# Optimization experiments

Measured on AMD Instinct MI355X. Metric: run time of the kernel, lower is better.

Reference implementation:

```python
import jax, jax.numpy as jnp
import numpy as np

B, N, C, H = 16, 4096, 1024, 8
D = C // H  # head dim = 128
EPS = 1e-5


def layernorm(x, gamma, beta):
    mu = jnp.mean(x, axis=-1, keepdims=True)
    var = jnp.mean(jnp.square(x - mu), axis=-1, keepdims=True)
    return (x - mu) * jax.lax.rsqrt(var + EPS) * gamma + beta


def setup_inputs() -> dict:
    key = jax.random.key(0)
    ks = jax.random.split(key, 5)
    w_std = C ** -0.5
    return {
        "class_feature": jax.random.normal(ks[0], (1, 1, C), dtype=jnp.float32),
        "features": jax.random.normal(ks[1], (B, N, C), dtype=jnp.float32),
        "q_gamma": jnp.ones((C,), jnp.float32),
        "q_beta": jnp.zeros((C,), jnp.float32),
        "Wq": jax.random.normal(ks[2], (C, C), dtype=jnp.float32) * w_std,
        "kv_gamma": jnp.ones((C,), jnp.float32),
        "kv_beta": jnp.zeros((C,), jnp.float32),
        "Wkv": jax.random.normal(ks[3], (2 * C, C), dtype=jnp.float32) * w_std,
        "proj_W": jax.random.normal(ks[4], (C, C), dtype=jnp.float32) * w_std,
        "proj_b": jnp.zeros((C,), jnp.float32),
    }


def reference(class_feature, features, q_gamma, q_beta, Wq,
              kv_gamma, kv_beta, Wkv, proj_W, proj_b):
    b, n, c = features.shape
    scale = c ** -0.5  # NOTE: original scales by input_size^-0.5, not head_dim^-0.5
    cf = jnp.broadcast_to(class_feature, (b, 1, c))  # repeat(B,1,1)

    # q branch: LN + Linear (no bias); single query token per batch
    q = layernorm(cf, q_gamma, q_beta) @ Wq.T            # (B,1,C)
    q = q.reshape(b, H, D)                               # (B,H,D)

    # kv branch: LN + Linear -> split into k,v per head
    kv = layernorm(features, kv_gamma, kv_beta) @ Wkv.T  # (B,N,2C)
    kv = kv.reshape(b, n, 2, H, D)
    k = kv[:, :, 0]                                      # (B,N,H,D)
    v = kv[:, :, 1]                                      # (B,N,H,D)

    # single-query attention per head
    attn = jnp.einsum('bhd,bnhd->bhn', q * scale, k)     # (B,H,N)
    attn = jax.nn.softmax(attn, axis=-1)
    agg = jnp.einsum('bhn,bnhd->bhd', attn, v)           # (B,H,D)
    agg = agg.reshape(b, 1, c)

    return cf + agg @ proj_W.T + proj_b
```

## Files before the change

kernel.cpp:

```cpp
#include <hip/hip_runtime.h>
#include <math.h>


#define BB 16
#define NN 4096
#define CC 1024
#define HH 8
#define DD 128
#define CHUNKS 32
#define RPB 128
#define TPT 4
#define NT 32

constexpr float EPS_ = 1e-5f;
constexpr float SCALE_ = 0.03125f;

typedef float v2f __attribute__((ext_vector_type(2)));

__device__ __forceinline__ void pkfma(v2f& d, v2f a, v2f b) {
  asm("v_pk_fma_f32 %0, %1, %2, %0" : "+v"(d) : "v"(a), "v"(b));
}
__device__ __forceinline__ void pkadd(v2f& d, v2f a) {
  asm("v_pk_add_f32 %0, %1, %0" : "+v"(d) : "v"(a));
}
__device__ __forceinline__ v2f lo2(const float4& f) { return v2f{f.x, f.y}; }
__device__ __forceinline__ v2f hi2(const float4& f) { return v2f{f.z, f.w}; }

__device__ __forceinline__ float wsum(float v) {
#pragma unroll
  for (int o = 32; o; o >>= 1) v += __shfl_xor(v, o, 64);
  return v;
}

__device__ __forceinline__ float dpp_sum63(float v) {
  int t;
  t = __builtin_amdgcn_update_dpp(0, __float_as_int(v), 0x111, 0xf, 0xf, true);  v += __int_as_float(t);
  t = __builtin_amdgcn_update_dpp(0, __float_as_int(v), 0x112, 0xf, 0xf, true);  v += __int_as_float(t);
  t = __builtin_amdgcn_update_dpp(0, __float_as_int(v), 0x114, 0xf, 0xf, true);  v += __int_as_float(t);
  t = __builtin_amdgcn_update_dpp(0, __float_as_int(v), 0x118, 0xf, 0xf, true);  v += __int_as_float(t);
  t = __builtin_amdgcn_update_dpp(0, __float_as_int(v), 0x142, 0xa, 0xf, false); v += __int_as_float(t);
  t = __builtin_amdgcn_update_dpp(0, __float_as_int(v), 0x143, 0xc, 0xf, false); v += __int_as_float(t);
  return v;
}

__device__ __forceinline__ float rsum_u(float v) {
  return __int_as_float(__builtin_amdgcn_readlane(__float_as_int(dpp_sum63(v)), 63));
}

__device__ __forceinline__ float dot4(const float4& a, const float4& b) {
  return a.x * b.x + a.y * b.y + a.z * b.z + a.w * b.w;
}
__device__ __forceinline__ float sum4(const float4& a) {
  return (a.x + a.y) + (a.z + a.w);
}

__device__ __forceinline__ void bar_lgkm() {
  asm volatile("s_waitcnt lgkmcnt(0)" ::: "memory");
  __builtin_amdgcn_sched_barrier(0);
  __builtin_amdgcn_s_barrier();
  __builtin_amdgcn_sched_barrier(0);
}

__global__ __launch_bounds__(256) void k0b(const float* __restrict__ cf,
                                           const float* __restrict__ g,
                                           const float* __restrict__ be,
                                           const float* __restrict__ Wq,
                                           float* __restrict__ qvec) {
  __shared__ __align__(16) float lnbuf[CC];
  __shared__ float red[8];
  int t = threadIdx.x, lane = t & 63, wid = t >> 6;
  float x[4];
  float s = 0.f, s2 = 0.f;
#pragma unroll
  for (int j = 0; j < 4; ++j) {
    x[j] = cf[t * 4 + j];
    s += x[j];
    s2 += x[j] * x[j];
  }
  s = wsum(s);
  s2 = wsum(s2);
  if (lane == 0) { red[wid] = s; red[4 + wid] = s2; }
  __syncthreads();
  float S = red[0] + red[1] + red[2] + red[3];
  float S2 = red[4] + red[5] + red[6] + red[7];
  float mu = S * (1.f / CC);
  float rstd = rsqrtf(S2 * (1.f / CC) - mu * mu + EPS_);
#pragma unroll
  for (int j = 0; j < 4; ++j)
    lnbuf[t * 4 + j] = (x[j] - mu) * rstd * g[t * 4 + j] + be[t * 4 + j];
  __syncthreads();
  int j = blockIdx.x * 4 + wid;
  const float4* wr = (const float4*)(Wq + (size_t)j * CC);
  const float4* l4 = (const float4*)lnbuf;
  float a = 0.f;
#pragma unroll
  for (int k = 0; k < 4; ++k) a += dot4(wr[lane + 64 * k], l4[lane + 64 * k]);
  a = wsum(a);
  if (lane == 0) qvec[j] = a;
}

__global__ __launch_bounds__(256) void k0c(const float* __restrict__ qvec,
                                           const float* __restrict__ Wkv,
                                           const float* __restrict__ kvg,
                                           float* __restrict__ qW,
                                           float* __restrict__ qWg) {
  int h = blockIdx.x >> 4;
  int c0 = (blockIdx.x & 15) * 64;
  int t = threadIdx.x, cl = t & 63, g = t >> 6;
  float a = 0.f;
#pragma unroll 8
  for (int d = g * 32; d < g * 32 + 32; ++d)
    a += qvec[h * DD + d] * Wkv[((size_t)(h * DD + d)) * CC + c0 + cl];
  __shared__ float red[4][64];
  red[g][cl] = a;
  __syncthreads();
  if (t < 64) {
    float v = (red[0][t] + red[1][t] + red[2][t] + red[3][t]) * SCALE_;
    qW[h * CC + c0 + t] = v;
    qWg[h * CC + c0 + t] = v * kvg[c0 + t];
  }
}

__global__ __launch_bounds__(256, 2) void kfused(
    const float* __restrict__ x, const float* __restrict__ qWg,
    const float* __restrict__ qW, const float* __restrict__ kvb,
    float* __restrict__ part_s, float* __restrict__ part_meu) {
  __shared__ __align__(16) float xbuf[2][TPT * CC];
  __shared__ __align__(8) float mr_lds[2][TPT][2];

  const int t = threadIdx.x, lane = t & 63, wid = t >> 6;
  const int chunk = blockIdx.x, b = blockIdx.y;
  const int bc = b * CHUNKS + chunk;
  const int h0 = wid * 2;

  const float* gx = x + ((size_t)b * NN + (size_t)chunk * RPB) * CC;
  const int sl = wid * 256 + lane;

  float4 pf[4];
  {
    const float4* g0 = (const float4*)gx;
#pragma unroll
    for (int k = 0; k < 4; ++k) pf[k] = g0[sl + 64 * k];
  }

  float4 qw0[4], qw1[4];
  {
    const float4* a0 = (const float4*)(qWg + (size_t)h0 * CC);
    const float4* a1 = (const float4*)(qWg + (size_t)(h0 + 1) * CC);
#pragma unroll
    for (int k = 0; k < 4; ++k) {
      qw0[k] = a0[lane + 64 * k];
      qw1[k] = a1[lane + 64 * k];
    }
  }
  float qs0, qs1, qb0, qb1;
  {
    float s0 = 0.f, s1 = 0.f, t0 = 0.f, t1 = 0.f;
    const float4* w0 = (const float4*)(qW + (size_t)h0 * CC);
    const float4* w1 = (const float4*)(qW + (size_t)(h0 + 1) * CC);
    const float4* b4 = (const float4*)kvb;
#pragma unroll
    for (int k = 0; k < 4; ++k) {
      s0 += sum4(qw0[k]);
      s1 += sum4(qw1[k]);
      float4 bt = b4[lane + 64 * k];
      t0 += dot4(w0[lane + 64 * k], bt);
      t1 += dot4(w1[lane + 64 * k], bt);
    }
    qs0 = rsum_u(s0);
    qs1 = rsum_u(s1);
    qb0 = rsum_u(t0);
    qb1 = rsum_u(t1);
  }

  v2f acc0[8], acc1[8];
#pragma unroll
  for (int k = 0; k < 8; ++k) {
    acc0[k] = v2f{0.f, 0.f};
    acc1[k] = v2f{0.f, 0.f};
  }
  float e0 = 0.f, e1 = 0.f, un0 = 0.f, un1 = 0.f;

  for (int tl = 0; tl < NT; ++tl) {
    const int cur = tl & 1;
    {
      v2f sv = v2f{0.f, 0.f}, sv2 = v2f{0.f, 0.f};
#pragma unroll
      for (int k = 0; k < 4; ++k) {
        v2f plo = lo2(pf[k]), phi = hi2(pf[k]);
        pkadd(sv, plo);
        pkadd(sv, phi);
        pkfma(sv2, plo, plo);
        pkfma(sv2, phi, phi);
      }
      float ls = sv.x + sv.y;
      float ls2 = sv2.x + sv2.y;
      {
        float4* dst = (float4*)xbuf[cur];
#pragma unroll
        for (int k = 0; k < 4; ++k) dst[sl + 64 * k] = pf[k];
      }
      ls = dpp_sum63(ls);
      ls2 = dpp_sum63(ls2);
      if (lane == 63) {
        float mu = ls * (1.f / CC);
        float rs = rsqrtf(ls2 * (1.f / CC) - mu * mu + EPS_);
        mr_lds[cur][wid][0] = mu;
        mr_lds[cur][wid][1] = rs;
      }
    }
    if (tl + 1 < NT) {
      const float4* gn = (const float4*)(gx + (size_t)(tl + 1) * (TPT * CC));
#pragma unroll
      for (int k = 0; k < 4; ++k) pf[k] = gn[sl + 64 * k];
    }
    bar_lgkm();

    const float4* xb4 = (const float4*)xbuf[cur];
#pragma unroll
    for (int r = 0; r < TPT; ++r) {
      float4 x0 = xb4[r * 256 + lane];
      float4 x1 = xb4[r * 256 + lane + 64];
      float4 x2 = xb4[r * 256 + lane + 128];
      float4 x3 = xb4[r * 256 + lane + 192];
      v2f xl0 = lo2(x0), xh0 = hi2(x0), xl1 = lo2(x1), xh1 = hi2(x1);
      v2f xl2 = lo2(x2), xh2 = hi2(x2), xl3 = lo2(x3), xh3 = hi2(x3);
      v2f d0v = v2f{0.f, 0.f}, d1v = v2f{0.f, 0.f};
      pkfma(d0v, lo2(qw0[0]), xl0); pkfma(d0v, hi2(qw0[0]), xh0);
      pkfma(d0v, lo2(qw0[1]), xl1); pkfma(d0v, hi2(qw0[1]), xh1);
      pkfma(d0v, lo2(qw0[2]), xl2); pkfma(d0v, hi2(qw0[2]), xh2);
      pkfma(d0v, lo2(qw0[3]), xl3); pkfma(d0v, hi2(qw0[3]), xh3);
      pkfma(d1v, lo2(qw1[0]), xl0); pkfma(d1v, hi2(qw1[0]), xh0);
      pkfma(d1v, lo2(qw1[1]), xl1); pkfma(d1v, hi2(qw1[1]), xh1);
      pkfma(d1v, lo2(qw1[2]), xl2); pkfma(d1v, hi2(qw1[2]), xh2);
      pkfma(d1v, lo2(qw1[3]), xl3); pkfma(d1v, hi2(qw1[3]), xh3);
      float D0 = rsum_u(d0v.x + d0v.y);
      float D1 = rsum_u(d1v.x + d1v.y);
      float2 mr = *(const float2*)mr_lds[cur][r];
      float mu = mr.x, rs = mr.y;
      float l0 = fminf(rs * (D0 - mu * qs0) + qb0, 75.f);
      float l1 = fminf(rs * (D1 - mu * qs1) + qb1, 75.f);
      float p0 = __expf(l0), p1 = __expf(l1);
      float w0 = p0 * rs, w1 = p1 * rs;
      e0 += p0; e1 += p1;
      un0 += w0 * mu; un1 += w1 * mu;
      v2f w0v = v2f{w0, w0}, w1v = v2f{w1, w1};
      pkfma(acc0[0], w0v, xl0); pkfma(acc0[1], w0v, xh0);
      pkfma(acc0[2], w0v, xl1); pkfma(acc0[3], w0v, xh1);
      pkfma(acc0[4], w0v, xl2); pkfma(acc0[5], w0v, xh2);
      pkfma(acc0[6], w0v, xl3); pkfma(acc0[7], w0v, xh3);
      pkfma(acc1[0], w1v, xl0); pkfma(acc1[1], w1v, xh0);
      pkfma(acc1[2], w1v, xl1); pkfma(acc1[3], w1v, xh1);
      pkfma(acc1[4], w1v, xl2); pkfma(acc1[5], w1v, xh2);
      pkfma(acc1[6], w1v, xl3); pkfma(acc1[7], w1v, xh3);
    }
  }

  float4* p0 = (float4*)(part_s + ((size_t)bc * HH + h0) * CC);
  float4* p1 = (float4*)(part_s + ((size_t)bc * HH + h0 + 1) * CC);
#pragma unroll
  for (int k = 0; k < 4; ++k) {
    p0[64 * k + lane] = make_float4(acc0[2 * k].x, acc0[2 * k].y,
                                    acc0[2 * k + 1].x, acc0[2 * k + 1].y);
    p1[64 * k + lane] = make_float4(acc1[2 * k].x, acc1[2 * k].y,
                                    acc1[2 * k + 1].x, acc1[2 * k + 1].y);
  }
  if (lane == 0) {
    float* pm = part_meu + ((size_t)bc * HH + h0) * 2;
    pm[0] = e0; pm[1] = un0;
    pm[2] = e1; pm[3] = un1;
  }
}

__global__ __launch_bounds__(256) void kmerge(
    const float* __restrict__ part_s, const float* __restrict__ part_meu,
    const float* __restrict__ kvg, const float* __restrict__ kvb,
    float* __restrict__ s) {
  int h = blockIdx.x >> 2, q = blockIdx.x & 3, b = blockIdx.y;
  int col = q * 256 + threadIdx.x;
  float E = 0.f, UN = 0.f, a = 0.f;
  for (int ch = 0; ch < CHUNKS; ++ch) {
    const float* pm = part_meu + (((size_t)b * CHUNKS + ch) * HH + h) * 2;
    E += pm[0];
    UN += pm[1];
    a += part_s[(((size_t)b * CHUNKS + ch) * HH + h) * CC + col];
  }
  float inv = 1.f / E;
  s[((size_t)b * HH + h) * CC + col] = kvg[col] * (a - UN) * inv + kvb[col];
}

__global__ __launch_bounds__(256) void k5(const float* __restrict__ Wkv,
                                          const float* __restrict__ s,
                                          float* __restrict__ agg) {
  int lane = threadIdx.x & 63;
  int j = blockIdx.x * 4 + (threadIdx.x >> 6);
  int h = j >> 7;
  const float4* wr = (const float4*)(Wkv + ((size_t)(CC + j)) * CC);
  float4 wv[4];
#pragma unroll
  for (int k = 0; k < 4; ++k) wv[k] = wr[lane + 64 * k];
  for (int b = 0; b < BB; ++b) {
    const float4* s4 = (const float4*)(s + ((size_t)(b * HH + h)) * CC);
    float a = 0.f;
#pragma unroll
    for (int k = 0; k < 4; ++k) a += dot4(wv[k], s4[lane + 64 * k]);
    a = wsum(a);
    if (lane == 0) agg[b * CC + j] = a;
  }
}

__global__ __launch_bounds__(256) void k6(const float* __restrict__ pW,
                                          const float* __restrict__ agg,
                                          const float* __restrict__ cf,
                                          const float* __restrict__ pb,
                                          float* __restrict__ out) {
  int lane = threadIdx.x & 63;
  int j = blockIdx.x * 4 + (threadIdx.x >> 6);
  const float4* wr = (const float4*)(pW + (size_t)j * CC);
  float4 wv[4];
#pragma unroll
  for (int k = 0; k < 4; ++k) wv[k] = wr[lane + 64 * k];
  for (int b = 0; b < BB; ++b) {
    const float4* a4 = (const float4*)(agg + (size_t)b * CC);
    float a = 0.f;
#pragma unroll
    for (int k = 0; k < 4; ++k) a += dot4(wv[k], a4[lane + 64 * k]);
    a = wsum(a);
    if (lane == 0) out[b * CC + j] = cf[j] + a + pb[j];
  }
}

constexpr size_t WS_QVEC = 0;
constexpr size_t WS_QW   = 1024;
constexpr size_t WS_QWG  = 9216;
constexpr size_t WS_S    = 17408;
constexpr size_t WS_AGG  = 148480;
constexpr size_t WS_PMEU = 164864;
constexpr size_t WS_PART = 173056;

extern "C" void kernel_launch(void* const* d_in, const int* in_sizes, int n_in,
                              void* d_out, int out_size, void* d_ws, size_t ws_size,
                              hipStream_t stream) {
  const float* cf = (const float*)d_in[0];
  const float* x = (const float*)d_in[1];
  const float* qg = (const float*)d_in[2];
  const float* qb = (const float*)d_in[3];
  const float* Wq = (const float*)d_in[4];
  const float* kvg = (const float*)d_in[5];
  const float* kvb = (const float*)d_in[6];
  const float* Wkv = (const float*)d_in[7];
  const float* pW = (const float*)d_in[8];
  const float* pb = (const float*)d_in[9];
  float* ws = (float*)d_ws;
  float* out = (float*)d_out;

  k0b<<<256, 256, 0, stream>>>(cf, qg, qb, Wq, ws + WS_QVEC);
  k0c<<<128, 256, 0, stream>>>(ws + WS_QVEC, Wkv, kvg, ws + WS_QW, ws + WS_QWG);
  kfused<<<dim3(CHUNKS, BB), 256, 0, stream>>>(x, ws + WS_QWG, ws + WS_QW, kvb,
                                               ws + WS_PART, ws + WS_PMEU);
  kmerge<<<dim3(HH * 4, BB), 256, 0, stream>>>(ws + WS_PART, ws + WS_PMEU, kvg, kvb,
                                               ws + WS_S);
  k5<<<256, 256, 0, stream>>>(Wkv, ws + WS_S, ws + WS_AGG);
  k6<<<256, 256, 0, stream>>>(pW, ws + WS_AGG, cf, pb, out);
}
```

Measured before the change: 102.4 us.

## Stage feature tiles via direct global-to-LDS loads and double tile rows

Replaces the register prefetch followed by an LDS store with __builtin_amdgcn_global_load_lds, which DMAs each 8-row tile straight into the alternate LDS buffer. Tile height goes from 4 to 8 rows, so there are half as many iterations and barriers, and each wave now computes LayerNorm statistics for two rows read back from LDS. The aim is to free VGPRs and the VALU/LDS-write work spent copying the tile, and to cut per-tile sync overhead. In exchange, LDS use doubles to 64KB per block, which could hurt the two-blocks-per-CU occupancy, and the vmcnt wait at the top of each iteration may expose load latency.

```diff
diff --git a/kernel.cpp b/kernel.cpp
--- a/kernel.cpp
+++ b/kernel.cpp
@@ -9,8 +9,8 @@
 #define DD 128
 #define CHUNKS 32
 #define RPB 128
-#define TPT 4
-#define NT 32
+#define TPT 8
+#define NT 16
 
 constexpr float EPS_ = 1e-5f;
 constexpr float SCALE_ = 0.03125f;
@@ -59,6 +59,26 @@
   __builtin_amdgcn_sched_barrier(0);
   __builtin_amdgcn_s_barrier();
   __builtin_amdgcn_sched_barrier(0);
+}
+
+__device__ __forceinline__ void wait_vm0() {
+  asm volatile("s_waitcnt vmcnt(0)" ::: "memory");
+  __builtin_amdgcn_sched_barrier(0);
+}
+
+__device__ __forceinline__ void stage_tile(const float* gsrc, float* lbase,
+                                           int ra, int lane) {
+#pragma unroll
+  for (int r = 0; r < 2; ++r) {
+#pragma unroll
+    for (int k = 0; k < 4; ++k) {
+      const char* g = (const char*)gsrc + (ra + r) * 4096 + k * 1024 + lane * 16;
+      char* l = (char*)lbase + (ra + r) * 4096 + k * 1024;
+      __builtin_amdgcn_global_load_lds(
+          (const __attribute__((address_space(1))) void*)g,
+          (__attribute__((address_space(3))) void*)l, 16, 0, 0);
+    }
+  }
 }
 
 __global__ __launch_bounds__(256) void k0b(const float* __restrict__ cf,
@@ -132,16 +152,10 @@
   const int chunk = blockIdx.x, b = blockIdx.y;
   const int bc = b * CHUNKS + chunk;
   const int h0 = wid * 2;
+  const int ra = wid * 2;
 
   const float* gx = x + ((size_t)b * NN + (size_t)chunk * RPB) * CC;
-  const int sl = wid * 256 + lane;
-
-  float4 pf[4];
-  {
-    const float4* g0 = (const float4*)gx;
-#pragma unroll
-    for (int k = 0; k < 4; ++k) pf[k] = g0[sl + 64 * k];
-  }
+  stage_tile(gx, xbuf[0], ra, lane);
 
   float4 qw0[4], qw1[4];
   {
@@ -183,38 +197,43 @@
 
   for (int tl = 0; tl < NT; ++tl) {
     const int cur = tl & 1;
+
+    wait_vm0();
+
     {
-      v2f sv = v2f{0.f, 0.f}, sv2 = v2f{0.f, 0.f};
+      const float4* xb4 = (const float4*)xbuf[cur];
+      v2f svA = v2f{0.f, 0.f}, svA2 = v2f{0.f, 0.f};
+      v2f svB = v2f{0.f, 0.f}, svB2 = v2f{0.f, 0.f};
 #pragma unroll
       for (int k = 0; k < 4; ++k) {
-        v2f plo = lo2(pf[k]), phi = hi2(pf[k]);
-        pkadd(sv, plo);
-        pkadd(sv, phi);
-        pkfma(sv2, plo, plo);
-        pkfma(sv2, phi, phi);
+        float4 xa = xb4[ra * 256 + lane + 64 * k];
+        float4 xb = xb4[(ra + 1) * 256 + lane + 64 * k];
+        v2f al = lo2(xa), ah = hi2(xa), bl = lo2(xb), bh = hi2(xb);
+        pkadd(svA, al); pkadd(svA, ah);
+        pkfma(svA2, al, al); pkfma(svA2, ah, ah);
+        pkadd(svB, bl); pkadd(svB, bh);
+        pkfma(svB2, bl, bl); pkfma(svB2, bh, bh);
       }
-      float ls = sv.x + sv.y;
-      float ls2 = sv2.x + sv2.y;
-      {
-        float4* dst = (float4*)xbuf[cur];
-#pragma unroll
-        for (int k = 0; k < 4; ++k) dst[sl + 64 * k] = pf[k];
+      float lsA = dpp_sum63(svA.x + svA.y);
+      float lsA2 = dpp_sum63(svA2.x + svA2.y);
+      float lsB = dpp_sum63(svB.x + svB.y);
+      float lsB2 = dpp_sum63(svB2.x + svB2.y);
+      if (lane == 63) {
+        float muA = lsA * (1.f / CC);
+        float rsA = rsqrtf(lsA2 * (1.f / CC) - muA * muA + EPS_);
+        float muB = lsB * (1.f / CC);
+        float rsB = rsqrtf(lsB2 * (1.f / CC) - muB * muB + EPS_);
+        mr_lds[cur][ra][0] = muA;
+        mr_lds[cur][ra][1] = rsA;
+        mr_lds[cur][ra + 1][0] = muB;
+        mr_lds[cur][ra + 1][1] = rsB;
       }
-      ls = dpp_sum63(ls);
-      ls2 = dpp_sum63(ls2);
-      if (lane == 63) {
-        float mu = ls * (1.f / CC);
-        float rs = rsqrtf(ls2 * (1.f / CC) - mu * mu + EPS_);
-        mr_lds[cur][wid][0] = mu;
-        mr_lds[cur][wid][1] = rs;
-      }
-    }
-    if (tl + 1 < NT) {
-      const float4* gn = (const float4*)(gx + (size_t)(tl + 1) * (TPT * CC));
-#pragma unroll
-      for (int k = 0; k < 4; ++k) pf[k] = gn[sl + 64 * k];
-    }
+    }
+
     bar_lgkm();
+
+    if (tl + 1 < NT)
+      stage_tile(gx + (size_t)(tl + 1) * (TPT * CC), xbuf[cur ^ 1], ra, lane);
 
     const float4* xb4 = (const float4*)xbuf[cur];
 #pragma unroll
```

Result: slower. 107.8 us (+5.3%).

## Stage feature tiles via direct global-to-LDS loads with triple-buffered pipeline

Applied to the files above, without the earlier changes.

Replaces the register-staged prefetch (global load into registers, then LDS store) with global_load_lds DMA straight into shared memory. Shared buffers go from two to three so tile tl+2 can be in flight while tile tl is computed, with vmcnt waits as the guard. The LayerNorm statistics are now read back from LDS rather than taken from registers. This removes the register round-trip and the LDS store instructions and frees VGPRs. In exchange it uses more LDS per block, which may affect the two-blocks-per-CU occupancy, and it depends on correct vmcnt accounting.

```diff
diff --git a/kernel.cpp b/kernel.cpp
--- a/kernel.cpp
+++ b/kernel.cpp
@@ -59,6 +59,27 @@
   __builtin_amdgcn_sched_barrier(0);
   __builtin_amdgcn_s_barrier();
   __builtin_amdgcn_sched_barrier(0);
+}
+
+__device__ __forceinline__ void wait_vm4() {
+  asm volatile("s_waitcnt vmcnt(4)" ::: "memory");
+  __builtin_amdgcn_sched_barrier(0);
+}
+__device__ __forceinline__ void wait_vm0() {
+  asm volatile("s_waitcnt vmcnt(0)" ::: "memory");
+  __builtin_amdgcn_sched_barrier(0);
+}
+
+__device__ __forceinline__ void stage_tile(const float* gsrc, float* lbase,
+                                           int wid, int lane) {
+#pragma unroll
+  for (int k = 0; k < 4; ++k) {
+    const char* g = (const char*)gsrc + wid * 4096 + k * 1024 + lane * 16;
+    char* l = (char*)lbase + wid * 4096 + k * 1024;
+    __builtin_amdgcn_global_load_lds(
+        (const __attribute__((address_space(1))) void*)g,
+        (__attribute__((address_space(3))) void*)l, 16, 0, 0);
+  }
 }
 
 __global__ __launch_bounds__(256) void k0b(const float* __restrict__ cf,
@@ -125,8 +146,8 @@
     const float* __restrict__ x, const float* __restrict__ qWg,
     const float* __restrict__ qW, const float* __restrict__ kvb,
     float* __restrict__ part_s, float* __restrict__ part_meu) {
-  __shared__ __align__(16) float xbuf[2][TPT * CC];
-  __shared__ __align__(8) float mr_lds[2][TPT][2];
+  __shared__ __align__(16) float xbuf[3][TPT * CC];
+  __shared__ __align__(8) float mr_lds[3][TPT][2];
 
   const int t = threadIdx.x, lane = t & 63, wid = t >> 6;
   const int chunk = blockIdx.x, b = blockIdx.y;
@@ -134,14 +155,8 @@
   const int h0 = wid * 2;
 
   const float* gx = x + ((size_t)b * NN + (size_t)chunk * RPB) * CC;
-  const int sl = wid * 256 + lane;
-
-  float4 pf[4];
-  {
-    const float4* g0 = (const float4*)gx;
-#pragma unroll
-    for (int k = 0; k < 4; ++k) pf[k] = g0[sl + 64 * k];
-  }
+  stage_tile(gx, xbuf[0], wid, lane);
+  stage_tile(gx + TPT * CC, xbuf[1], wid, lane);
 
   float4 qw0[4], qw1[4];
   {
@@ -181,27 +196,24 @@
   }
   float e0 = 0.f, e1 = 0.f, un0 = 0.f, un1 = 0.f;
 
+  int cur = 0;
   for (int tl = 0; tl < NT; ++tl) {
-    const int cur = tl & 1;
+    if (tl < NT - 1) wait_vm4(); else wait_vm0();
+
     {
+      const float4* xr = (const float4*)xbuf[cur] + wid * 256;
       v2f sv = v2f{0.f, 0.f}, sv2 = v2f{0.f, 0.f};
 #pragma unroll
       for (int k = 0; k < 4; ++k) {
-        v2f plo = lo2(pf[k]), phi = hi2(pf[k]);
-        pkadd(sv, plo);
-        pkadd(sv, phi);
-        pkfma(sv2, plo, plo);
-        pkfma(sv2, phi, phi);
+        float4 xa = xr[lane + 64 * k];
+        v2f al = lo2(xa), ah = hi2(xa);
+        pkadd(sv, al);
+        pkadd(sv, ah);
+        pkfma(sv2, al, al);
+        pkfma(sv2, ah, ah);
       }
-      float ls = sv.x + sv.y;
-      float ls2 = sv2.x + sv2.y;
-      {
-        float4* dst = (float4*)xbuf[cur];
-#pragma unroll
-        for (int k = 0; k < 4; ++k) dst[sl + 64 * k] = pf[k];
-      }
-      ls = dpp_sum63(ls);
-      ls2 = dpp_sum63(ls2);
+      float ls = dpp_sum63(sv.x + sv.y);
+      float ls2 = dpp_sum63(sv2.x + sv2.y);
       if (lane == 63) {
         float mu = ls * (1.f / CC);
         float rs = rsqrtf(ls2 * (1.f / CC) - mu * mu + EPS_);
@@ -209,12 +221,14 @@
         mr_lds[cur][wid][1] = rs;
       }
     }
-    if (tl + 1 < NT) {
-      const float4* gn = (const float4*)(gx + (size_t)(tl + 1) * (TPT * CC));
-#pragma unroll
-      for (int k = 0; k < 4; ++k) pf[k] = gn[sl + 64 * k];
-    }
+
     bar_lgkm();
+
+    if (tl + 2 < NT) {
+      int slot = cur + 2;
+      if (slot >= 3) slot -= 3;
+      stage_tile(gx + (size_t)(tl + 2) * (TPT * CC), xbuf[slot], wid, lane);
+    }
 
     const float4* xb4 = (const float4*)xbuf[cur];
 #pragma unroll
@@ -254,6 +268,7 @@
       pkfma(acc1[4], w1v, xl2); pkfma(acc1[5], w1v, xh2);
       pkfma(acc1[6], w1v, xl3); pkfma(acc1[7], w1v, xh3);
     }
+    cur = (cur + 1 == 3) ? 0 : cur + 1;
   }
 
   float4* p0 = (float4*)(part_s + ((size_t)bc * HH + h0) * CC);
```

Measured after the change: 106.3 us. +3.8%, slower.

## Fuse chunk merge with V-projection into one kernel using LDS

Applied to the files above, without the earlier changes.

Merges the per-chunk partial sums kernel and the Wkv value-projection kernel into one launch per (head, batch). The merged s vector stays in shared memory instead of going through global workspace, which removes one launch and the s round trip. In exchange, each block re-reads its head's 128 Wkv rows, so V weights are read 16 times (once per batch) instead of once, and the grid shrinks to 128 blocks. The reduction also switches to a DPP-based sum whose result lands in lane 63.

```diff
diff --git a/kernel.cpp b/kernel.cpp
--- a/kernel.cpp
+++ b/kernel.cpp
@@ -272,40 +272,51 @@
   }
 }
 
-__global__ __launch_bounds__(256) void kmerge(
+__global__ __launch_bounds__(256) void kmerge5(
     const float* __restrict__ part_s, const float* __restrict__ part_meu,
     const float* __restrict__ kvg, const float* __restrict__ kvb,
-    float* __restrict__ s) {
-  int h = blockIdx.x >> 2, q = blockIdx.x & 3, b = blockIdx.y;
-  int col = q * 256 + threadIdx.x;
-  float E = 0.f, UN = 0.f, a = 0.f;
+    const float* __restrict__ Wkv, float* __restrict__ agg) {
+  __shared__ __align__(16) float s_lds[CC];
+  const int h = blockIdx.x, b = blockIdx.y;
+  const int t = threadIdx.x, lane = t & 63, wid = t >> 6;
+
+  float E = 0.f, UN = 0.f;
   for (int ch = 0; ch < CHUNKS; ++ch) {
     const float* pm = part_meu + (((size_t)b * CHUNKS + ch) * HH + h) * 2;
     E += pm[0];
     UN += pm[1];
-    a += part_s[(((size_t)b * CHUNKS + ch) * HH + h) * CC + col];
   }
   float inv = 1.f / E;
-  s[((size_t)b * HH + h) * CC + col] = kvg[col] * (a - UN) * inv + kvb[col];
-}
-
-__global__ __launch_bounds__(256) void k5(const float* __restrict__ Wkv,
-                                          const float* __restrict__ s,
-                                          float* __restrict__ agg) {
-  int lane = threadIdx.x & 63;
-  int j = blockIdx.x * 4 + (threadIdx.x >> 6);
-  int h = j >> 7;
-  const float4* wr = (const float4*)(Wkv + ((size_t)(CC + j)) * CC);
-  float4 wv[4];
-#pragma unroll
-  for (int k = 0; k < 4; ++k) wv[k] = wr[lane + 64 * k];
-  for (int b = 0; b < BB; ++b) {
-    const float4* s4 = (const float4*)(s + ((size_t)(b * HH + h)) * CC);
+
+  float4 a4 = make_float4(0.f, 0.f, 0.f, 0.f);
+  for (int ch = 0; ch < CHUNKS; ++ch) {
+    const float4* ps =
+        (const float4*)(part_s + (((size_t)b * CHUNKS + ch) * HH + h) * CC);
+    float4 v = ps[t];
+    a4.x += v.x; a4.y += v.y; a4.z += v.z; a4.w += v.w;
+  }
+  float4 g4 = ((const float4*)kvg)[t];
+  float4 b4 = ((const float4*)kvb)[t];
+  float4 sv;
+  sv.x = g4.x * (a4.x - UN) * inv + b4.x;
+  sv.y = g4.y * (a4.y - UN) * inv + b4.y;
+  sv.z = g4.z * (a4.z - UN) * inv + b4.z;
+  sv.w = g4.w * (a4.w - UN) * inv + b4.w;
+  ((float4*)s_lds)[t] = sv;
+  __syncthreads();
+
+  const float4* s4 = (const float4*)s_lds;
+  float4 lv[4];
+#pragma unroll
+  for (int k = 0; k < 4; ++k) lv[k] = s4[lane + 64 * k];
+  for (int i = 0; i < 32; ++i) {
+    int j = h * DD + wid * 32 + i;
+    const float4* wr = (const float4*)(Wkv + ((size_t)(CC + j)) * CC);
     float a = 0.f;
 #pragma unroll
-    for (int k = 0; k < 4; ++k) a += dot4(wv[k], s4[lane + 64 * k]);
-    a = wsum(a);
-    if (lane == 0) agg[b * CC + j] = a;
+    for (int k = 0; k < 4; ++k) a += dot4(wr[lane + 64 * k], lv[k]);
+    a = dpp_sum63(a);
+    if (lane == 63) agg[b * CC + j] = a;
   }
 }
 
@@ -333,10 +344,9 @@
 constexpr size_t WS_QVEC = 0;
 constexpr size_t WS_QW   = 1024;
 constexpr size_t WS_QWG  = 9216;
-constexpr size_t WS_S    = 17408;
-constexpr size_t WS_AGG  = 148480;
-constexpr size_t WS_PMEU = 164864;
-constexpr size_t WS_PART = 173056;
+constexpr size_t WS_AGG  = 17408;
+constexpr size_t WS_PMEU = 33792;
+constexpr size_t WS_PART = 41984;
 
 extern "C" void kernel_launch(void* const* d_in, const int* in_sizes, int n_in,
                               void* d_out, int out_size, void* d_ws, size_t ws_size,
@@ -358,8 +368,7 @@
   k0c<<<128, 256, 0, stream>>>(ws + WS_QVEC, Wkv, kvg, ws + WS_QW, ws + WS_QWG);
   kfused<<<dim3(CHUNKS, BB), 256, 0, stream>>>(x, ws + WS_QWG, ws + WS_QW, kvb,
                                                ws + WS_PART, ws + WS_PMEU);
-  kmerge<<<dim3(HH * 4, BB), 256, 0, stream>>>(ws + WS_PART, ws + WS_PMEU, kvg, kvb,
-                                               ws + WS_S);
-  k5<<<256, 256, 0, stream>>>(Wkv, ws + WS_S, ws + WS_AGG);
+  kmerge5<<<dim3(HH, BB), 256, 0, stream>>>(ws + WS_PART, ws + WS_PMEU, kvg, kvb,
+                                            Wkv, ws + WS_AGG);
   k6<<<256, 256, 0, stream>>>(pW, ws + WS_AGG, cf, pb, out);
 }
```

Result: slower. 109.7 us (+7.1%).
